# Kernel optimization log

Measured on AMD Instinct MI355X. Metric: run time of the kernel, lower is better.

The kernel has to match this reference:

```python
import jax, jax.numpy as jnp
import numpy as np

B, N, V, T = 16, 1024, 4096, 8


def _lsa(cost):
    """Jonker-Volgenant linear sum assignment on a square [n,n] cost matrix.
    Returns (row_ind, col_ind) minimizing cost[row, col].sum(). Equivalent to
    scipy.optimize.linear_sum_assignment for square matrices."""
    n = cost.shape[0]
    INF = np.inf
    u = np.zeros(n + 1)
    v = np.zeros(n + 1)
    p = np.zeros(n + 1, dtype=np.int64)    # p[j] = row assigned to column j (1-based)
    way = np.zeros(n + 1, dtype=np.int64)
    for i in range(1, n + 1):
        p[0] = i
        j0 = 0
        minv = np.full(n + 1, INF)
        used = np.zeros(n + 1, dtype=bool)
        while True:
            used[j0] = True
            i0 = p[j0]
            free = ~used
            free[0] = False
            cur = cost[i0 - 1, :] - u[i0] - v[1:]
            upd = free[1:] & (cur < minv[1:])
            minv[1:][upd] = cur[upd]
            way[1:][upd] = j0
            j1 = int(np.argmin(np.where(free[1:], minv[1:], INF))) + 1
            delta = minv[j1]
            u[p[used]] += delta
            v[used] -= delta
            minv[~used] -= delta
            j0 = j1
            if p[j0] == 0:
                break
        while j0:
            j1 = way[j0]
            p[j0] = p[j1]
            j0 = j1
    col_of_row = np.empty(n, dtype=np.int64)
    for j in range(1, n + 1):
        col_of_row[p[j] - 1] = j - 1
    return np.arange(n), col_of_row


def _compute_assignment(lp_np, gt_np, types_np, mask_np):
    """For each (sample, node_type) group of masked nodes, Hungarian-match
    positions to gt tokens. Returns flat (batch_idx, pos_idx, tok_idx) of all
    matched pairs. Mirrors the original type-wise padded loop (k==1 is identity)."""
    Bn = lp_np.shape[0]
    b_l, p_l, t_l = [], [], []
    for t in np.unique(types_np):
        for b in range(Bn):
            idx = np.nonzero((types_np[b] == t) & mask_np[b])[0]
            k = idx.size
            if k == 0:
                continue
            g = gt_np[b, idx]
            if k == 1:
                r = np.zeros(1, dtype=np.int64)
                c = np.zeros(1, dtype=np.int64)
            else:
                cost = -lp_np[b, idx][:, g]  # [k, k]
                r, c = _lsa(cost)
            b_l.append(np.full(k, b, dtype=np.int64))
            p_l.append(idx[r])
            t_l.append(g[c])
    return np.concatenate(b_l), np.concatenate(p_l), np.concatenate(t_l)


def setup_inputs() -> dict:
    key = jax.random.key(0)
    k1, k2, k3, k4 = jax.random.split(key, 4)
    logits = jax.random.normal(k1, (B, N, V), dtype=jnp.float32)
    gt_tokens = jax.random.randint(k2, (B, N), 0, V)
    node_types = jax.random.randint(k3, (B, N), 0, T)
    mask_positions = jax.random.randint(k4, (B, N), 0, 2).astype(bool)
    return {"logits": logits, "gt_tokens": gt_tokens,
            "node_types": node_types, "mask_positions": mask_positions}


def reference(logits, gt_tokens, node_types, mask_positions):
    # Dense log-softmax over vocab (the memory-bound bulk of the op).
    log_probs = jax.nn.log_softmax(logits, axis=-1)
    # Assignment is computed on detached values (matches .detach() in original).
    b_idx, p_idx, t_idx = _compute_assignment(
        np.asarray(jax.lax.stop_gradient(log_probs)),
        np.asarray(gt_tokens), np.asarray(node_types), np.asarray(mask_positions))
    total = b_idx.shape[0]  # total matched (masked) tokens
    sel = log_probs[jnp.asarray(b_idx), jnp.asarray(p_idx), jnp.asarray(t_idx)]
    # avg_loss = sum_b(loss_per_sample*count)/total_count == sum of matched NLL / total
    return -sel.sum() / jnp.asarray(total, sel.dtype)
```

## Files before the change

### kernel.cpp

```cpp
#include <hip/hip_runtime.h>
#include <math.h>

#define BB 16
#define NN 1024
#define VV 4096
#define TT 8
#define NG (BB*TT)
#define KMAX 124
#define STRIDE 124

__device__ __forceinline__ float wave_max(float v){
  #pragma unroll
  for (int off = 32; off; off >>= 1) v = fmaxf(v, __shfl_down(v, off));
  return v;
}
__device__ __forceinline__ float wave_sum(float v){
  #pragma unroll
  for (int off = 32; off; off >>= 1) v += __shfl_down(v, off);
  return v;
}

__device__ __forceinline__ unsigned fkey(float f){
  unsigned b = __float_as_uint(f);
  return b ^ ((unsigned)((int)b >> 31) | 0x80000000u);
}
__device__ __forceinline__ float inv_fkey(unsigned u){
  unsigned b = (u & 0x80000000u) ? (u ^ 0x80000000u) : ~u;
  return __uint_as_float(b);
}

__device__ __forceinline__ unsigned dpp_min64(unsigned x){
  unsigned t;
  t = (unsigned)__builtin_amdgcn_update_dpp(-1, (int)x, 0x111, 0xF, 0xF, false); x = x < t ? x : t;
  t = (unsigned)__builtin_amdgcn_update_dpp(-1, (int)x, 0x112, 0xF, 0xF, false); x = x < t ? x : t;
  t = (unsigned)__builtin_amdgcn_update_dpp(-1, (int)x, 0x114, 0xF, 0xF, false); x = x < t ? x : t;
  t = (unsigned)__builtin_amdgcn_update_dpp(-1, (int)x, 0x118, 0xF, 0xF, false); x = x < t ? x : t;
  t = (unsigned)__builtin_amdgcn_update_dpp(-1, (int)x, 0x142, 0xF, 0xF, false); x = x < t ? x : t;
  t = (unsigned)__builtin_amdgcn_update_dpp(-1, (int)x, 0x143, 0xF, 0xF, false); x = x < t ? x : t;
  return x;
}

__global__ __launch_bounds__(64) void k_prep(const unsigned char* __restrict__ raw,
                                             const int* __restrict__ types,
                                             const int* __restrict__ gt,
                                             int* __restrict__ mnorm,
                                             int* __restrict__ idxg,
                                             int* __restrict__ gtkg,
                                             int* __restrict__ kcnt){
  int g = blockIdx.x, b = g >> 3, t = g & 7, lane = threadIdx.x;
  int local = 0;
  for (int i = lane; i < 4096; i += 64)
    local |= raw[4*i+1] | raw[4*i+2] | raw[4*i+3];
  bool bool_layout = (__ballot(local != 0) != 0ull);
  const int* rawi = (const int*)raw;
  for (int r = 0; r < 2; r++){
    int o = g*128 + r*64 + lane;
    int v = bool_layout ? (int)raw[o] : rawi[o];
    mnorm[o] = (v != 0);
  }
  int base = 0;
  for (int r = 0; r < NN/64; r++){
    int pos = r*64 + lane, o = b*NN + pos;
    int mv = bool_layout ? (int)raw[o] : rawi[o];
    bool pred = (types[o] == t) && (mv != 0);
    unsigned long long ball = __ballot(pred);
    int dst = base + __popcll(ball & ((1ull << lane) - 1ull));
    if (pred && dst < KMAX){
      idxg[g*KMAX + dst] = pos;
      gtkg[g*KMAX + dst] = gt[o];
    }
    base += __popcll(ball);
  }
  if (lane == 0) kcnt[g] = (base > KMAX) ? KMAX : base;
}

__global__ __launch_bounds__(256) void k_lse(const float* __restrict__ logits,
                                             const int* __restrict__ mask,
                                             float* __restrict__ lse){
  int row = blockIdx.x;
  if (mask[row] == 0) return;
  const float4* x = (const float4*)(logits + (size_t)row * VV);
  int tid = threadIdx.x;
  float4 a = x[tid], b = x[tid+256], c = x[tid+512], d = x[tid+768];
  float m = fmaxf(fmaxf(fmaxf(fmaxf(a.x,a.y),fmaxf(a.z,a.w)),
                        fmaxf(fmaxf(b.x,b.y),fmaxf(b.z,b.w))),
                  fmaxf(fmaxf(fmaxf(c.x,c.y),fmaxf(c.z,c.w)),
                        fmaxf(fmaxf(d.x,d.y),fmaxf(d.z,d.w))));
  __shared__ float red[8];
  float wm = wave_max(m);
  int wid = tid >> 6;
  if ((tid & 63) == 0) red[wid] = wm;
  __syncthreads();
  if (tid == 0) red[4] = fmaxf(fmaxf(red[0],red[1]), fmaxf(red[2],red[3]));
  __syncthreads();
  float M = red[4];
  float s = __expf(a.x-M)+__expf(a.y-M)+__expf(a.z-M)+__expf(a.w-M)
          + __expf(b.x-M)+__expf(b.y-M)+__expf(b.z-M)+__expf(b.w-M)
          + __expf(c.x-M)+__expf(c.y-M)+__expf(c.z-M)+__expf(c.w-M)
          + __expf(d.x-M)+__expf(d.y-M)+__expf(d.z-M)+__expf(d.w-M);
  float ws = wave_sum(s);
  __syncthreads();
  if ((tid & 63) == 0) red[wid] = ws;
  __syncthreads();
  if (tid == 0) lse[row] = M + __logf(red[0]+red[1]+red[2]+red[3]);
}

__global__ __launch_bounds__(64) void k_jv(const float* __restrict__ logits,
                                           const int* __restrict__ idxg,
                                           const int* __restrict__ gtkg,
                                           const int* __restrict__ kcnt,
                                           float* __restrict__ gval){
  __shared__ float Cm[KMAX*STRIDE];
  __shared__ float u_l[KMAX+1];
  __shared__ int   p_l[KMAX+1];
  __shared__ int   way_l[KMAX+1];
  __shared__ int   rowown[KMAX];
  __shared__ int   listA[KMAX];
  __shared__ int   listB[KMAX];
  int g = blockIdx.x, b = g >> 3, lane = threadIdx.x;
  int k = kcnt[g];
  if (k > KMAX) k = KMAX;
  if (k == 0){ if (lane == 0) gval[g] = 0.f; return; }

  int col0 = lane + 1, col1 = lane + 65;
  bool a0 = (col0 <= k), a1 = (col1 <= k);
  int gc0 = a0 ? gtkg[g*KMAX + lane]      : 0;
  int gc1 = a1 ? gtkg[g*KMAX + lane + 64] : 0;

  if (lane < k)      way_l[lane]    = idxg[g*KMAX + lane];
  if (lane+64 < k)   way_l[lane+64] = idxg[g*KMAX + lane + 64];
  u_l[col0] = 0.f; p_l[col0] = 0;
  if (col1 <= KMAX){ u_l[col1] = 0.f; p_l[col1] = 0; }
  if (lane == 0){ u_l[0] = 0.f; p_l[0] = 0; }
  rowown[lane] = -1;
  if (lane + 64 < KMAX) rowown[lane+64] = -1;
  __syncthreads();

  const size_t rowbase = (size_t)b * NN;
  for (int i = 0; i < k; i += 4){
    int r0 = i, r1 = min(i+1, k-1), r2 = min(i+2, k-1), r3 = min(i+3, k-1);
    const float* q0 = logits + (rowbase + way_l[r0]) * VV;
    const float* q1 = logits + (rowbase + way_l[r1]) * VV;
    const float* q2 = logits + (rowbase + way_l[r2]) * VV;
    const float* q3 = logits + (rowbase + way_l[r3]) * VV;
    float x00 = q0[gc0], x01 = q0[gc1];
    float x10 = q1[gc0], x11 = q1[gc1];
    float x20 = q2[gc0], x21 = q2[gc1];
    float x30 = q3[gc0], x31 = q3[gc1];
    Cm[r0*STRIDE + lane] = -x00; Cm[r0*STRIDE + 64 + lane] = -x01;
    Cm[r1*STRIDE + lane] = -x10; Cm[r1*STRIDE + 64 + lane] = -x11;
    Cm[r2*STRIDE + lane] = -x20; Cm[r2*STRIDE + 64 + lane] = -x21;
    Cm[r3*STRIDE + lane] = -x30; Cm[r3*STRIDE + 64 + lane] = -x31;
  }
  __syncthreads();

  float v0 = 0.f, v1 = 0.f;
  int ra0 = -1, ra1 = -1;
  if (a0){ float m = INFINITY; int rm = 0;
    for (int i = 0; i < k; i++){ float c = Cm[i*STRIDE + lane]; if (c < m){ m = c; rm = i; } }
    v0 = m; ra0 = rm; }
  if (a1){ float m = INFINITY; int rm = 0;
    for (int i = 0; i < k; i++){ float c = Cm[i*STRIDE + 64 + lane]; if (c < m){ m = c; rm = i; } }
    v1 = m; ra1 = rm; }
  if (a0){ if (atomicCAS(&rowown[ra0], -1, col0) == -1) p_l[col0] = ra0 + 1; }
  if (a1){ if (atomicCAS(&rowown[ra1], -1, col1) == -1) p_l[col1] = ra1 + 1; }
  __syncthreads();

  bool f0 = (lane < k)    && (rowown[lane]    == -1);
  bool f1 = (lane+64 < k) && (rowown[lane+64] == -1);
  unsigned long long B0 = __ballot(f0), B1 = __ballot(f1);
  unsigned long long lm = (1ull << lane) - 1ull;
  int n0 = __popcll(B0);
  if (f0) listA[__popcll(B0 & lm)]      = lane + 1;
  if (f1) listA[n0 + __popcll(B1 & lm)] = lane + 65;
  int nCur = n0 + __popcll(B1);
  __syncthreads();

  int* curL = listA; int* nxtL = listB;
  for (int pass = 0; pass < 2; pass++){
    int nNxt = 0;
    for (int fr = 0; fr < nCur; fr++){
      int row = curL[fr];
      int off = (row - 1) * STRIDE;
      float rc0 = a0 ? (Cm[off + lane]      - v0) : INFINITY;
      float rc1 = a1 ? (Cm[off + 64 + lane] - v1) : INFINITY;
      unsigned k0 = fkey(rc0), k1 = fkey(rc1);
      unsigned kk = k0 < k1 ? k0 : k1;
      unsigned m1 = (unsigned)__builtin_amdgcn_readlane((int)dpp_min64(kk), 63);
      int cand = (k0 == m1) ? col0 : ((k1 == m1) ? col1 : 0);
      unsigned long long bl1 = __ballot(cand != 0);
      int ow1 = __ffsll(bl1) - 1;
      int j1 = __builtin_amdgcn_readlane(cand, ow1);
      float u1 = inv_fkey(m1);
      unsigned k0b = (col0 == j1) ? 0xFFFFFFFFu : k0;
      unsigned k1b = (col1 == j1) ? 0xFFFFFFFFu : k1;
      unsigned kkb = k0b < k1b ? k0b : k1b;
      unsigned m2 = (unsigned)__builtin_amdgcn_readlane((int)dpp_min64(kkb), 63);
      float u2 = inv_fkey(m2);
      int jt = j1;
      if (u1 < u2){
        if (col0 == j1) v0 -= (u2 - u1);
        if (col1 == j1) v1 -= (u2 - u1);
      } else {
        int own1 = p_l[j1];
        if (own1 != 0){
          int cand2 = (k0b == m2) ? col0 : ((k1b == m2) ? col1 : 0);
          unsigned long long bl2 = __ballot(cand2 != 0);
          int ow2 = __ffsll(bl2) - 1;
          jt = __builtin_amdgcn_readlane(cand2, ow2);
        }
      }
      int iprev = p_l[jt];
      if (lane == 0){ p_l[jt] = row; u_l[row] = u2; }
      if (iprev != 0){ if (lane == 0) nxtL[nNxt] = iprev; nNxt++; }
      __syncthreads();
    }
    int* tmp = curL; curL = nxtL; nxtL = tmp;
    nCur = nNxt;
  }

  for (int fr = 0; fr < nCur; fr++){
    int irow = curL[fr];
    int rp0 = a0 ? p_l[col0] : 0;
    int rp1 = a1 ? p_l[col1] : 0;
    float rpu0 = (rp0 > 0) ? u_l[rp0] : 0.f;
    float rpu1 = (rp1 > 0) ? u_l[rp1] : 0.f;
    int off = (irow - 1) * STRIDE;
    float dist0 = a0 ? (Cm[off + lane]      - v0) : INFINITY;
    float dist1 = a1 ? (Cm[off + 64 + lane] - v1) : INFINITY;
    int way0 = 0, way1 = 0;
    bool used0 = false, used1 = false;
    int j_end; float delta_end;
    while (true){
      unsigned q0 = (a0 && !used0) ? ((fkey(dist0) & 0xFFFFFF80u) | (unsigned)(col0-1)) : 0xFFFFFFFFu;
      unsigned q1 = (a1 && !used1) ? ((fkey(dist1) & 0xFFFFFF80u) | (unsigned)(col1-1)) : 0xFFFFFFFFu;
      unsigned key = q0 < q1 ? q0 : q1;
      unsigned kmin = (unsigned)__builtin_amdgcn_readlane((int)dpp_min64(key), 63);
      int j1 = (int)(kmin & 127u) + 1;
      int owner = (j1-1) & 63, slot = (j1-1) >> 6, addr = owner << 2;
      float dsel  = slot ? dist1 : dist0;
      int   psel  = slot ? rp1   : rp0;
      float pusel = slot ? rpu1  : rpu0;
      int di  = __builtin_amdgcn_ds_bpermute(addr, __float_as_int(dsel));
      int pi  = __builtin_amdgcn_ds_bpermute(addr, psel);
      int pui = __builtin_amdgcn_ds_bpermute(addr, __float_as_int(pusel));
      float delta = __int_as_float(di);
      int i0 = __builtin_amdgcn_readfirstlane(pi);
      used0 |= (j1 == col0);
      used1 |= (j1 == col1);
      if (i0 == 0){ j_end = j1; delta_end = delta; break; }
      float base = delta - __int_as_float(pui);
      int o2 = (i0 - 1) * STRIDE;
      float c0 = Cm[o2 + lane];
      float c1 = Cm[o2 + 64 + lane];
      float nd0 = base + c0 - v0;
      float nd1 = base + c1 - v1;
      if (a0 && !used0 && (nd0 < dist0)){ dist0 = nd0; way0 = j1; }
      if (a1 && !used1 && (nd1 < dist1)){ dist1 = nd1; way1 = j1; }
    }
    if (used0){ float adj = delta_end - dist0; v0 -= adj; u_l[rp0] = rpu0 + adj; }
    if (used1){ float adj = delta_end - dist1; v1 -= adj; u_l[rp1] = rpu1 + adj; }
    if (lane == 0) u_l[irow] = delta_end;
    if (a0) way_l[col0] = way0;
    if (a1) way_l[col1] = way1;
    __syncthreads();
    int j0 = j_end;
    while (true){
      int jw = way_l[j0];
      int pr = p_l[jw];
      int pw = (jw == 0) ? irow : pr;
      if (lane == 0) p_l[j0] = pw;
      if (jw == 0) break;
      j0 = jw;
    }
    __syncthreads();
  }

  __syncthreads();
  float acc = 0.f;
  if (a0) acc += Cm[(p_l[col0]-1)*STRIDE + lane];
  if (a1) acc += Cm[(p_l[col1]-1)*STRIDE + 64 + lane];
  acc = wave_sum(acc);
  if (lane == 0) gval[g] = -acc;
}

__global__ __launch_bounds__(256) void k_final(const float* __restrict__ lse,
                                               const int* __restrict__ mask,
                                               const float* __restrict__ gval,
                                               float* __restrict__ out){
  __shared__ double sd[256];
  __shared__ double sg[256];
  __shared__ int    si[256];
  int tid = threadIdx.x;
  double s = 0.0, gs = 0.0; int c = 0;
  for (int i = tid; i < BB*NN; i += 256)
    if (mask[i]){ s += (double)lse[i]; c++; }
  for (int i = tid; i < NG; i += 256) gs += (double)gval[i];
  sd[tid] = s; sg[tid] = gs; si[tid] = c;
  __syncthreads();
  for (int off = 128; off; off >>= 1){
    if (tid < off){ sd[tid] += sd[tid+off]; sg[tid] += sg[tid+off]; si[tid] += si[tid+off]; }
    __syncthreads();
  }
  if (tid == 0) out[0] = (float)((sd[0] - sg[0]) / (double)si[0]);
}

extern "C" void kernel_launch(void* const* d_in, const int* in_sizes, int n_in,
                              void* d_out, int out_size, void* d_ws, size_t ws_size,
                              hipStream_t stream) {
  const float* logits = (const float*)d_in[0];
  const int*   gt     = (const int*)d_in[1];
  const int*   types  = (const int*)d_in[2];
  const unsigned char* maskraw = (const unsigned char*)d_in[3];
  float* out = (float*)d_out;

  char* w = (char*)d_ws;
  float* lse   = (float*)w;  w += (size_t)BB*NN*4;
  int*   mnorm = (int*)w;    w += (size_t)BB*NN*4;
  int*   idxg  = (int*)w;    w += (size_t)NG*KMAX*4;
  int*   gtkg  = (int*)w;    w += (size_t)NG*KMAX*4;
  int*   kcnt  = (int*)w;    w += 1024;
  float* gval  = (float*)w;  w += 1024;

  k_prep <<<NG,     64, 0, stream>>>(maskraw, types, gt, mnorm, idxg, gtkg, kcnt);
  k_lse  <<<BB*NN, 256, 0, stream>>>(logits, mnorm, lse);
  k_jv   <<<NG,     64, 0, stream>>>(logits, idxg, gtkg, kcnt, gval);
  k_final<<<1,     256, 0, stream>>>(lse, mnorm, gval, out);
}
```

Before: 500.1 us.

## Fold prep kernel into LSE and JV kernels, use readlane broadcast

```diff
diff --git a/kernel.cpp b/kernel.cpp
--- a/kernel.cpp
+++ b/kernel.cpp
@@ -40,47 +40,22 @@
   return x;
 }
 
-__global__ __launch_bounds__(64) void k_prep(const unsigned char* __restrict__ raw,
-                                             const int* __restrict__ types,
-                                             const int* __restrict__ gt,
-                                             int* __restrict__ mnorm,
-                                             int* __restrict__ idxg,
-                                             int* __restrict__ gtkg,
-                                             int* __restrict__ kcnt){
-  int g = blockIdx.x, b = g >> 3, t = g & 7, lane = threadIdx.x;
-  int local = 0;
-  for (int i = lane; i < 4096; i += 64)
-    local |= raw[4*i+1] | raw[4*i+2] | raw[4*i+3];
-  bool bool_layout = (__ballot(local != 0) != 0ull);
-  const int* rawi = (const int*)raw;
-  for (int r = 0; r < 2; r++){
-    int o = g*128 + r*64 + lane;
-    int v = bool_layout ? (int)raw[o] : rawi[o];
-    mnorm[o] = (v != 0);
-  }
-  int base = 0;
-  for (int r = 0; r < NN/64; r++){
-    int pos = r*64 + lane, o = b*NN + pos;
-    int mv = bool_layout ? (int)raw[o] : rawi[o];
-    bool pred = (types[o] == t) && (mv != 0);
-    unsigned long long ball = __ballot(pred);
-    int dst = base + __popcll(ball & ((1ull << lane) - 1ull));
-    if (pred && dst < KMAX){
-      idxg[g*KMAX + dst] = pos;
-      gtkg[g*KMAX + dst] = gt[o];
-    }
-    base += __popcll(ball);
-  }
-  if (lane == 0) kcnt[g] = (base > KMAX) ? KMAX : base;
-}
-
 __global__ __launch_bounds__(256) void k_lse(const float* __restrict__ logits,
-                                             const int* __restrict__ mask,
+                                             const unsigned char* __restrict__ raw,
                                              float* __restrict__ lse){
   int row = blockIdx.x;
-  if (mask[row] == 0) return;
+  int tid = threadIdx.x;
+  __shared__ int probe_nz;
+  if (tid == 0) probe_nz = 0;
+  __syncthreads();
+  uchar4 pv = ((const uchar4*)raw)[tid];
+  if (pv.y | pv.z | pv.w) atomicOr(&probe_nz, 1);
+  __syncthreads();
+  bool bool_layout = (probe_nz != 0);
+  int mv = bool_layout ? (int)raw[row] : ((const int*)raw)[row];
+  if (mv == 0){ if (tid == 0) lse[row] = 0.f; return; }
+
   const float4* x = (const float4*)(logits + (size_t)row * VV);
-  int tid = threadIdx.x;
   float4 a = x[tid], b = x[tid+256], c = x[tid+512], d = x[tid+768];
   float m = fmaxf(fmaxf(fmaxf(fmaxf(a.x,a.y),fmaxf(a.z,a.w)),
                         fmaxf(fmaxf(b.x,b.y),fmaxf(b.z,b.w))),
@@ -106,9 +81,10 @@
 }
 
 __global__ __launch_bounds__(64) void k_jv(const float* __restrict__ logits,
-                                           const int* __restrict__ idxg,
-                                           const int* __restrict__ gtkg,
-                                           const int* __restrict__ kcnt,
+                                           const int* __restrict__ types,
+                                           const int* __restrict__ gt,
+                                           const unsigned char* __restrict__ raw,
+                                           int* __restrict__ kcnt,
                                            float* __restrict__ gval){
   __shared__ float Cm[KMAX*STRIDE];
   __shared__ float u_l[KMAX+1];
@@ -117,18 +93,34 @@
   __shared__ int   rowown[KMAX];
   __shared__ int   listA[KMAX];
   __shared__ int   listB[KMAX];
-  int g = blockIdx.x, b = g >> 3, lane = threadIdx.x;
-  int k = kcnt[g];
-  if (k > KMAX) k = KMAX;
+  int g = blockIdx.x, b = g >> 3, t = g & 7, lane = threadIdx.x;
+  unsigned long long lm = (1ull << lane) - 1ull;
+
+  int local = 0;
+  const uchar4* r4 = (const uchar4*)raw;
+  #pragma unroll
+  for (int r = 0; r < 4; r++){ uchar4 u = r4[lane + 64*r]; local |= (u.y | u.z | u.w); }
+  bool bool_layout = (__ballot(local != 0) != 0ull);
+  const int* rawi = (const int*)raw;
+  int base = 0;
+  for (int r = 0; r < NN/64; r++){
+    int pos = r*64 + lane, o = b*NN + pos;
+    int mv = bool_layout ? (int)raw[o] : rawi[o];
+    bool pred = (types[o] == t) && (mv != 0);
+    unsigned long long ball = __ballot(pred);
+    int dst = base + __popcll(ball & lm);
+    if (pred && dst < KMAX){ way_l[dst] = pos; listA[dst] = gt[o]; }
+    base += __popcll(ball);
+  }
+  int k = (base > KMAX) ? KMAX : base;
+  if (lane == 0) kcnt[g] = k;
   if (k == 0){ if (lane == 0) gval[g] = 0.f; return; }
 
   int col0 = lane + 1, col1 = lane + 65;
   bool a0 = (col0 <= k), a1 = (col1 <= k);
-  int gc0 = a0 ? gtkg[g*KMAX + lane]      : 0;
-  int gc1 = a1 ? gtkg[g*KMAX + lane + 64] : 0;
-
-  if (lane < k)      way_l[lane]    = idxg[g*KMAX + lane];
-  if (lane+64 < k)   way_l[lane+64] = idxg[g*KMAX + lane + 64];
+  int gc0 = a0 ? listA[lane]      : 0;
+  int gc1 = a1 ? listA[lane + 64] : 0;
+
   u_l[col0] = 0.f; p_l[col0] = 0;
   if (col1 <= KMAX){ u_l[col1] = 0.f; p_l[col1] = 0; }
   if (lane == 0){ u_l[0] = 0.f; p_l[0] = 0; }
@@ -137,20 +129,19 @@
   __syncthreads();
 
   const size_t rowbase = (size_t)b * NN;
-  for (int i = 0; i < k; i += 4){
-    int r0 = i, r1 = min(i+1, k-1), r2 = min(i+2, k-1), r3 = min(i+3, k-1);
-    const float* q0 = logits + (rowbase + way_l[r0]) * VV;
-    const float* q1 = logits + (rowbase + way_l[r1]) * VV;
-    const float* q2 = logits + (rowbase + way_l[r2]) * VV;
-    const float* q3 = logits + (rowbase + way_l[r3]) * VV;
-    float x00 = q0[gc0], x01 = q0[gc1];
-    float x10 = q1[gc0], x11 = q1[gc1];
-    float x20 = q2[gc0], x21 = q2[gc1];
-    float x30 = q3[gc0], x31 = q3[gc1];
-    Cm[r0*STRIDE + lane] = -x00; Cm[r0*STRIDE + 64 + lane] = -x01;
-    Cm[r1*STRIDE + lane] = -x10; Cm[r1*STRIDE + 64 + lane] = -x11;
-    Cm[r2*STRIDE + lane] = -x20; Cm[r2*STRIDE + 64 + lane] = -x21;
-    Cm[r3*STRIDE + lane] = -x30; Cm[r3*STRIDE + 64 + lane] = -x31;
+  for (int i = 0; i < k; i += 8){
+    float xs0[8], xs1[8]; int rr[8];
+    #pragma unroll
+    for (int s = 0; s < 8; s++){
+      int r = i + s; r = (r < k) ? r : (k - 1); rr[s] = r;
+      const float* q = logits + (rowbase + way_l[r]) * VV;
+      xs0[s] = q[gc0]; xs1[s] = q[gc1];
+    }
+    #pragma unroll
+    for (int s = 0; s < 8; s++){
+      Cm[rr[s]*STRIDE + lane]      = -xs0[s];
+      Cm[rr[s]*STRIDE + 64 + lane] = -xs1[s];
+    }
   }
   __syncthreads();
 
@@ -169,7 +160,6 @@
   bool f0 = (lane < k)    && (rowown[lane]    == -1);
   bool f1 = (lane+64 < k) && (rowown[lane+64] == -1);
   unsigned long long B0 = __ballot(f0), B1 = __ballot(f1);
-  unsigned long long lm = (1ull << lane) - 1ull;
   int n0 = __popcll(B0);
   if (f0) listA[__popcll(B0 & lm)]      = lane + 1;
   if (f1) listA[n0 + __popcll(B1 & lm)] = lane + 65;
@@ -177,7 +167,7 @@
   __syncthreads();
 
   int* curL = listA; int* nxtL = listB;
-  for (int pass = 0; pass < 2; pass++){
+  for (int pass = 0; pass < 3; pass++){
     int nNxt = 0;
     for (int fr = 0; fr < nCur; fr++){
       int row = curL[fr];
@@ -237,24 +227,22 @@
       unsigned key = q0 < q1 ? q0 : q1;
       unsigned kmin = (unsigned)__builtin_amdgcn_readlane((int)dpp_min64(key), 63);
       int j1 = (int)(kmin & 127u) + 1;
-      int owner = (j1-1) & 63, slot = (j1-1) >> 6, addr = owner << 2;
+      int owner = (j1-1) & 63, slot = (j1-1) >> 6;
       float dsel  = slot ? dist1 : dist0;
       int   psel  = slot ? rp1   : rp0;
       float pusel = slot ? rpu1  : rpu0;
-      int di  = __builtin_amdgcn_ds_bpermute(addr, __float_as_int(dsel));
-      int pi  = __builtin_amdgcn_ds_bpermute(addr, psel);
-      int pui = __builtin_amdgcn_ds_bpermute(addr, __float_as_int(pusel));
-      float delta = __int_as_float(di);
-      int i0 = __builtin_amdgcn_readfirstlane(pi);
+      float delta = __uint_as_float((unsigned)__builtin_amdgcn_readlane(__float_as_int(dsel), owner));
+      int   i0    = __builtin_amdgcn_readlane(psel, owner);
+      float pu    = __uint_as_float((unsigned)__builtin_amdgcn_readlane(__float_as_int(pusel), owner));
       used0 |= (j1 == col0);
       used1 |= (j1 == col1);
       if (i0 == 0){ j_end = j1; delta_end = delta; break; }
-      float base = delta - __int_as_float(pui);
+      float bse = delta - pu;
       int o2 = (i0 - 1) * STRIDE;
       float c0 = Cm[o2 + lane];
       float c1 = Cm[o2 + 64 + lane];
-      float nd0 = base + c0 - v0;
-      float nd1 = base + c1 - v1;
+      float nd0 = bse + c0 - v0;
+      float nd1 = bse + c1 - v1;
       if (a0 && !used0 && (nd0 < dist0)){ dist0 = nd0; way0 = j1; }
       if (a1 && !used1 && (nd1 < dist1)){ dist1 = nd1; way1 = j1; }
     }
@@ -285,7 +273,7 @@
 }
 
 __global__ __launch_bounds__(256) void k_final(const float* __restrict__ lse,
-                                               const int* __restrict__ mask,
+                                               const int* __restrict__ kcnt,
                                                const float* __restrict__ gval,
                                                float* __restrict__ out){
   __shared__ double sd[256];
@@ -293,9 +281,8 @@
   __shared__ int    si[256];
   int tid = threadIdx.x;
   double s = 0.0, gs = 0.0; int c = 0;
-  for (int i = tid; i < BB*NN; i += 256)
-    if (mask[i]){ s += (double)lse[i]; c++; }
-  for (int i = tid; i < NG; i += 256) gs += (double)gval[i];
+  for (int i = tid; i < BB*NN; i += 256) s += (double)lse[i];
+  for (int i = tid; i < NG; i += 256){ gs += (double)gval[i]; c += kcnt[i]; }
   sd[tid] = s; sg[tid] = gs; si[tid] = c;
   __syncthreads();
   for (int off = 128; off; off >>= 1){
@@ -315,15 +302,11 @@
   float* out = (float*)d_out;
 
   char* w = (char*)d_ws;
-  float* lse   = (float*)w;  w += (size_t)BB*NN*4;
-  int*   mnorm = (int*)w;    w += (size_t)BB*NN*4;
-  int*   idxg  = (int*)w;    w += (size_t)NG*KMAX*4;
-  int*   gtkg  = (int*)w;    w += (size_t)NG*KMAX*4;
-  int*   kcnt  = (int*)w;    w += 1024;
-  float* gval  = (float*)w;  w += 1024;
-
-  k_prep <<<NG,     64, 0, stream>>>(maskraw, types, gt, mnorm, idxg, gtkg, kcnt);
-  k_lse  <<<BB*NN, 256, 0, stream>>>(logits, mnorm, lse);
-  k_jv   <<<NG,     64, 0, stream>>>(logits, idxg, gtkg, kcnt, gval);
-  k_final<<<1,     256, 0, stream>>>(lse, mnorm, gval, out);
-}
+  float* lse  = (float*)w;  w += (size_t)BB*NN*4;
+  int*   kcnt = (int*)w;    w += 1024;
+  float* gval = (float*)w;  w += 1024;
+
+  k_lse  <<<BB*NN, 256, 0, stream>>>(logits, maskraw, lse);
+  k_jv   <<<NG,     64, 0, stream>>>(logits, types, gt, maskraw, kcnt, gval);
+  k_final<<<1,     256, 0, stream>>>(lse, kcnt, gval, out);
+}
```

After: 457.6 us. 1.09x faster.
